# Performance work log

Measured on AMD Instinct MI355X. Metric: run time of the kernel, lower is better.

## Reference

```python
import jax, jax.numpy as jnp
import numpy as np

N_NODES = 100000
N_EDGES = 1600000
D = 128


def setup_inputs() -> dict:
    key = jax.random.key(0)
    ks = jax.random.split(key, 8)
    s = lambda fan_in: 1.0 / np.sqrt(fan_in)
    return {
        "node_feature": jax.random.normal(ks[0], (N_NODES, D), dtype=jnp.float32),
        "src": jax.random.randint(ks[1], (N_EDGES,), 0, N_NODES),
        "dst": jax.random.randint(ks[2], (N_EDGES,), 0, N_NODES),
        "W1": jax.random.normal(ks[3], (2 * D, D), dtype=jnp.float32) * s(2 * D),
        "b1": jnp.zeros((D,), dtype=jnp.float32),
        "W2": jax.random.normal(ks[4], (D, D), dtype=jnp.float32) * s(D),
        "b2": jnp.zeros((D,), dtype=jnp.float32),
        "W3": jax.random.normal(ks[5], (D, D), dtype=jnp.float32) * s(D),
        "b3": jnp.zeros((D,), dtype=jnp.float32),
    }


def reference(node_feature, src, dst, W1, b1, W2, b2, W3, b3):
    n_nodes = node_feature.shape[0]
    # message: gather src node features over edges  [E, D]
    msg = node_feature[src]
    # reduce: sum messages into destination nodes   [N, D]
    agg = jax.ops.segment_sum(msg, dst, num_segments=n_nodes)
    # apply: concat(aggregated, own) -> MLP         [N, 2D] -> [N, D]
    inp = jnp.concatenate([agg, node_feature], axis=-1)
    h = jax.nn.relu(inp @ W1 + b1)
    h = jax.nn.relu(h @ W2 + b2)
    return h @ W3 + b3
```

## Files before the change

kernel.cpp:

```cpp
#include <hip/hip_runtime.h>

#define NNODES 100000
#define NEDGES 1600000
#define DD 128
#define BM 32
#define NBUCK 98
#define NBLK_MLP (NNODES / BM)
#define CAP 32
#define CAPB 20480
#define BIN1_WGS 200
#define BIN1_EPW 8192

#define WS_GCUR 100000
#define WS_BBASE 100128
#define WS_OFFS 100352
#define WS_ESRC 201216

#define WT1HI 0
#define WT1LO 32768
#define WT2HI 65536
#define WT2LO 81920
#define WT3HI 98304
#define WT3LO 114688

typedef __attribute__((ext_vector_type(8))) short short8;
typedef __attribute__((ext_vector_type(4))) float f32x4;

__device__ __forceinline__ void bf16_split(float x, ushort& hi, ushort& lo) {
  unsigned u = __float_as_uint(x);
  ushort h = (ushort)((u + 0x7FFFu + ((u >> 16) & 1u)) >> 16);
  float r = x - __uint_as_float(((unsigned)h) << 16);
  unsigned v = __float_as_uint(r);
  ushort l = (ushort)((v + 0x7FFFu + ((v >> 16) & 1u)) >> 16);
  hi = h;
  lo = l;
}

__device__ __forceinline__ void split8(const float4 v0, const float4 v1,
                                       short8& hi, short8& lo) {
  float x[8] = {v0.x, v0.y, v0.z, v0.w, v1.x, v1.y, v1.z, v1.w};
#pragma unroll
  for (int j = 0; j < 8; ++j) {
    ushort h, l;
    bf16_split(x[j], h, l);
    hi[j] = (short)h;
    lo[j] = (short)l;
  }
}

__global__ __launch_bounds__(256) void bin1_kernel(const int* __restrict__ src,
                                                   const int* __restrict__ dst,
                                                   int* __restrict__ gcur,
                                                   unsigned* __restrict__ ebuf) {
  __shared__ unsigned stage[NBUCK][CAP];
  __shared__ int scnt[NBUCK];
  const int t = threadIdx.x;
  for (int i = t; i < NBUCK; i += 256) scnt[i] = 0;
  __syncthreads();
  const int e0 = blockIdx.x * BIN1_EPW;
  for (int r = 0; r < BIN1_EPW / 1024; ++r) {
    unsigned item[4];
    int buck[4];
    int pend[4];
#pragma unroll
    for (int j = 0; j < 4; ++j) {
      pend[j] = 0;
      int e = e0 + r * 1024 + j * 256 + t;
      if (e < NEDGES) {
        int d = dst[e];
        int s = src[e];
        buck[j] = d >> 10;
        item[j] = ((unsigned)(d & 1023) << 17) | (unsigned)s;
        int p = atomicAdd(&scnt[buck[j]], 1);
        if (p < CAP)
          stage[buck[j]][p] = item[j];
        else
          pend[j] = 1;
      }
    }
    int pendLeft;
    do {
      __syncthreads();
      if (t < NBUCK && scnt[t] >= CAP) {
        int base = t * CAPB + atomicAdd(&gcur[t], CAP);
        for (int q = 0; q < CAP; ++q) ebuf[base + q] = stage[t][q];
        scnt[t] = 0;
      }
      __syncthreads();
      int mypend = 0;
#pragma unroll
      for (int j = 0; j < 4; ++j) {
        if (pend[j]) {
          int p = atomicAdd(&scnt[buck[j]], 1);
          if (p < CAP) {
            stage[buck[j]][p] = item[j];
            pend[j] = 0;
          } else {
            mypend = 1;
          }
        }
      }
      pendLeft = __syncthreads_count(mypend);
    } while (pendLeft > 0);
  }
  __syncthreads();
  if (t < NBUCK) {
    int n = scnt[t];
    if (n > 0) {
      int base = t * CAPB + atomicAdd(&gcur[t], n);
      for (int q = 0; q < n; ++q) ebuf[base + q] = stage[t][q];
    }
  }
}

__global__ __launch_bounds__(128) void bscan_kernel(const int* __restrict__ gcur,
                                                    int* __restrict__ bbase,
                                                    int* __restrict__ offs) {
  __shared__ int s[128];
  const int t = threadIdx.x;
  int v = (t < NBUCK) ? gcur[t] : 0;
  s[t] = v;
  __syncthreads();
  for (int off = 1; off < 128; off <<= 1) {
    int u = (t >= off) ? s[t - off] : 0;
    __syncthreads();
    s[t] += u;
    __syncthreads();
  }
  if (t < NBUCK) bbase[t] = s[t] - v;
  if (t == NBUCK - 1) offs[NNODES] = s[t];
}

__global__ __launch_bounds__(1024) void bucket_csr_kernel(const unsigned* __restrict__ ebuf,
                                                          const int* __restrict__ gcur,
                                                          const int* __restrict__ bbase,
                                                          int* __restrict__ offs,
                                                          int* __restrict__ esrc) {
  __shared__ int h[1024];
  __shared__ int cur[1024];
  const int t = threadIdx.x;
  const int c = blockIdx.x;
  const int n = gcur[c];
  const unsigned* eb = ebuf + c * CAPB;
  h[t] = 0;
  __syncthreads();
  for (int i = t; i < n; i += 1024) atomicAdd(&h[eb[i] >> 17], 1);
  __syncthreads();
  int v = h[t];
  for (int off = 1; off < 1024; off <<= 1) {
    int u = (t >= off) ? h[t - off] : 0;
    __syncthreads();
    h[t] += u;
    __syncthreads();
  }
  int excl = h[t] - v + bbase[c];
  int node = (c << 10) + t;
  if (node < NNODES) offs[node] = excl;
  cur[t] = excl;
  __syncthreads();
  for (int i = t; i < n; i += 1024) {
    unsigned e = eb[i];
    int p = atomicAdd(&cur[e >> 17], 1);
    esrc[p] = (int)(e & 0x1FFFFu);
  }
}

__global__ __launch_bounds__(256) void wprep_kernel(const float* __restrict__ W1,
                                                    const float* __restrict__ W2,
                                                    const float* __restrict__ W3,
                                                    ushort* __restrict__ wt) {
  int tid = blockIdx.x * 256 + threadIdx.x;
  const float* W;
  int dstHi, dstLo, k, col;
  if (tid < 32768) {
    int j = tid & 7, l = (tid >> 3) & 63, tile = tid >> 9;
    int kk = tile & 7, c16 = tile >> 3;
    k = kk * 32 + (l >> 4) * 8 + j;
    col = c16 * 16 + (l & 15);
    W = W1;
    dstHi = WT1HI + tid;
    dstLo = WT1LO + tid;
  } else {
    int t2 = tid - 32768;
    int which = t2 >> 14;
    int t1 = t2 & 16383;
    int j = t1 & 7, l = (t1 >> 3) & 63, tile = t1 >> 9;
    int kk = tile & 3, c16 = tile >> 2;
    k = kk * 32 + (l >> 4) * 8 + j;
    col = c16 * 16 + (l & 15);
    W = which ? W3 : W2;
    dstHi = (which ? WT3HI : WT2HI) + t1;
    dstLo = (which ? WT3LO : WT2LO) + t1;
  }
  ushort hi, lo;
  bf16_split(W[k * DD + col], hi, lo);
  wt[dstHi] = hi;
  wt[dstLo] = lo;
}


template <int KT>
__device__ __forceinline__ void lds_ksteps(const ushort* Hh, const ushort* Hl,
                                           const ushort* __restrict__ WhiT,
                                           const ushort* __restrict__ WloT,
                                           int tileOff, int rb, int wc, int lane,
                                           int l15, int lhi, f32x4 acc[4]) {
#pragma unroll 2
  for (int kk = 0; kk < 4; ++kk) {
    int row = rb + l15;
    int byte = (row * 256 + kk * 64 + lhi * 16) ^ ((row & 7) << 4);
    short8 ahi = *(const short8*)((const char*)Hh + byte);
    short8 alo = *(const short8*)((const char*)Hl + byte);
#pragma unroll
    for (int ct = 0; ct < 4; ++ct) {
      int tb = ((wc * 4 + ct) * KT + tileOff + kk) * 512 + lane * 8;
      short8 bhi = *(const short8*)&WhiT[tb];
      short8 blo = *(const short8*)&WloT[tb];
      acc[ct] = __builtin_amdgcn_mfma_f32_16x16x32_bf16(ahi, bhi, acc[ct], 0, 0, 0);
      acc[ct] = __builtin_amdgcn_mfma_f32_16x16x32_bf16(ahi, blo, acc[ct], 0, 0, 0);
      acc[ct] = __builtin_amdgcn_mfma_f32_16x16x32_bf16(alo, bhi, acc[ct], 0, 0, 0);
    }
  }
}

__device__ __forceinline__ void l1_step(const float* __restrict__ srcb,
                                        const ushort* __restrict__ wt,
                                        int kkTile, int kOff, int rowA,
                                        int wc, int lane, int lhi,
                                        f32x4 acc[4]) {
  const float* p = srcb + rowA * DD + kOff + lhi * 8;
  float4 v0 = *(const float4*)p;
  float4 v1 = *(const float4*)(p + 4);
  short8 ahi, alo;
  split8(v0, v1, ahi, alo);
#pragma unroll
  for (int ct = 0; ct < 4; ++ct) {
    int tb = ((wc * 4 + ct) * 8 + kkTile) * 512 + lane * 8;
    short8 bhi = *(const short8*)&wt[WT1HI + tb];
    short8 blo = *(const short8*)&wt[WT1LO + tb];
    acc[ct] = __builtin_amdgcn_mfma_f32_16x16x32_bf16(ahi, bhi, acc[ct], 0, 0, 0);
    acc[ct] = __builtin_amdgcn_mfma_f32_16x16x32_bf16(ahi, blo, acc[ct], 0, 0, 0);
    acc[ct] = __builtin_amdgcn_mfma_f32_16x16x32_bf16(alo, bhi, acc[ct], 0, 0, 0);
  }
}

__device__ __forceinline__ void store_h(ushort* Hh, ushort* Hl,
                                        const float* __restrict__ b,
                                        int rb, int wc, int l15, int lhi,
                                        f32x4 acc[4]) {
#pragma unroll
  for (int ct = 0; ct < 4; ++ct) {
    int col = wc * 64 + ct * 16 + l15;
    float bias = b[col];
#pragma unroll
    for (int i = 0; i < 4; ++i) {
      int row = rb + lhi * 4 + i;
      float v = fmaxf(acc[ct][i] + bias, 0.f);
      ushort h, l;
      bf16_split(v, h, l);
      int byte = (row * 256 + col * 2) ^ ((row & 7) << 4);
      *(ushort*)((char*)Hh + byte) = h;
      *(ushort*)((char*)Hl + byte) = l;
    }
  }
}

__global__ __launch_bounds__(256, 8) void fused_kernel(const float* __restrict__ nf,
                                                       const int* __restrict__ offs,
                                                       const int* __restrict__ esrc,
                                                       const ushort* __restrict__ wt,
                                                       const float* __restrict__ b1,
                                                       const float* __restrict__ b2,
                                                       const float* __restrict__ b3,
                                                       float* __restrict__ out) {
  __shared__ ushort smem[8192];
  __shared__ int nextRow;
  ushort* Xhi = smem;
  ushort* Xlo = smem + 4096;

  const int t = threadIdx.x;
  const int lane = t & 63;
  const int w = t >> 6;
  const int rb = (w & 1) * 16;
  const int wc = w >> 1;
  const int l15 = lane & 15;
  const int lhi = lane >> 4;
  const int base = blockIdx.x * BM;

  if (t == 0) nextRow = 0;
  __syncthreads();

  {
    const int l32 = t & 31;
    const int col = l32 << 2;
    for (;;) {
      int r;
      if (l32 == 0) r = atomicAdd(&nextRow, 1);
      r = __shfl(r, 0, 32);
      if (r >= BM) break;
      const int node = base + r;
      float4 a0 = make_float4(0.f, 0.f, 0.f, 0.f);
      float4 a1 = make_float4(0.f, 0.f, 0.f, 0.f);
      float4 a2 = make_float4(0.f, 0.f, 0.f, 0.f);
      float4 a3 = make_float4(0.f, 0.f, 0.f, 0.f);
      const int beg = offs[node];
      const int end = offs[node + 1];
      int i = beg;
      int s0, s1, s2, s3;
      const bool have4 = (i + 3 < end);
      if (have4) {
        s0 = esrc[i]; s1 = esrc[i + 1]; s2 = esrc[i + 2]; s3 = esrc[i + 3];
      }
      for (; i + 7 < end; i += 4) {
        int n0 = esrc[i + 4], n1 = esrc[i + 5], n2 = esrc[i + 6], n3 = esrc[i + 7];
        float4 v0 = *(const float4*)&nf[s0 * DD + col];
        float4 v1 = *(const float4*)&nf[s1 * DD + col];
        float4 v2 = *(const float4*)&nf[s2 * DD + col];
        float4 v3 = *(const float4*)&nf[s3 * DD + col];
        a0.x += v0.x; a0.y += v0.y; a0.z += v0.z; a0.w += v0.w;
        a1.x += v1.x; a1.y += v1.y; a1.z += v1.z; a1.w += v1.w;
        a2.x += v2.x; a2.y += v2.y; a2.z += v2.z; a2.w += v2.w;
        a3.x += v3.x; a3.y += v3.y; a3.z += v3.z; a3.w += v3.w;
        s0 = n0; s1 = n1; s2 = n2; s3 = n3;
      }
      if (have4) {
        float4 v0 = *(const float4*)&nf[s0 * DD + col];
        float4 v1 = *(const float4*)&nf[s1 * DD + col];
        float4 v2 = *(const float4*)&nf[s2 * DD + col];
        float4 v3 = *(const float4*)&nf[s3 * DD + col];
        a0.x += v0.x; a0.y += v0.y; a0.z += v0.z; a0.w += v0.w;
        a1.x += v1.x; a1.y += v1.y; a1.z += v1.z; a1.w += v1.w;
        a2.x += v2.x; a2.y += v2.y; a2.z += v2.z; a2.w += v2.w;
        a3.x += v3.x; a3.y += v3.y; a3.z += v3.z; a3.w += v3.w;
        i += 4;
      }
      for (; i < end; ++i) {
        int s = esrc[i];
        float4 v0 = *(const float4*)&nf[s * DD + col];
        a0.x += v0.x; a0.y += v0.y; a0.z += v0.z; a0.w += v0.w;
      }
      a0.x += a1.x; a0.y += a1.y; a0.z += a1.z; a0.w += a1.w;
      a2.x += a3.x; a2.y += a3.y; a2.z += a3.z; a2.w += a3.w;
      a0.x += a2.x; a0.y += a2.y; a0.z += a2.z; a0.w += a2.w;
      ushort h0, h1, h2, h3, l0, l1, l2, l3;
      bf16_split(a0.x, h0, l0);
      bf16_split(a0.y, h1, l1);
      bf16_split(a0.z, h2, l2);
      bf16_split(a0.w, h3, l3);
      int byte = (r * 256 + col * 2) ^ ((r & 7) << 4);
      *(ushort4*)((char*)Xhi + byte) = make_ushort4(h0, h1, h2, h3);
      *(ushort4*)((char*)Xlo + byte) = make_ushort4(l0, l1, l2, l3);
    }
  }
  __syncthreads();

  const int rowG = base + rb + l15;
  const f32x4 z = {0.f, 0.f, 0.f, 0.f};
  f32x4 acc[4];

#pragma unroll
  for (int ct = 0; ct < 4; ++ct) acc[ct] = z;
  lds_ksteps<8>(Xhi, Xlo, wt + WT1HI, wt + WT1LO, 0, rb, wc, lane, l15, lhi, acc);
#pragma unroll 2
  for (int kk = 0; kk < 4; ++kk)
    l1_step(nf, wt, kk + 4, kk * 32, rowG, wc, lane, lhi, acc);
  __syncthreads();
  store_h(Xhi, Xlo, b1, rb, wc, l15, lhi, acc);
  __syncthreads();

#pragma unroll
  for (int ct = 0; ct < 4; ++ct) acc[ct] = z;
  lds_ksteps<4>(Xhi, Xlo, wt + WT2HI, wt + WT2LO, 0, rb, wc, lane, l15, lhi, acc);
  __syncthreads();
  store_h(Xhi, Xlo, b2, rb, wc, l15, lhi, acc);
  __syncthreads();

#pragma unroll
  for (int ct = 0; ct < 4; ++ct) acc[ct] = z;
  lds_ksteps<4>(Xhi, Xlo, wt + WT3HI, wt + WT3LO, 0, rb, wc, lane, l15, lhi, acc);
#pragma unroll
  for (int ct = 0; ct < 4; ++ct) {
    int col = wc * 64 + ct * 16 + l15;
    float bias = b3[col];
#pragma unroll
    for (int i = 0; i < 4; ++i) {
      int row = base + rb + lhi * 4 + i;
      out[row * DD + col] = acc[ct][i] + bias;
    }
  }
}

extern "C" void kernel_launch(void* const* d_in, const int* in_sizes, int n_in,
                              void* d_out, int out_size, void* d_ws, size_t ws_size,
                              hipStream_t stream) {
  const float* nf = (const float*)d_in[0];
  const int* src = (const int*)d_in[1];
  const int* dst = (const int*)d_in[2];
  const float* W1 = (const float*)d_in[3];
  const float* b1 = (const float*)d_in[4];
  const float* W2 = (const float*)d_in[5];
  const float* b2 = (const float*)d_in[6];
  const float* W3 = (const float*)d_in[7];
  const float* b3 = (const float*)d_in[8];
  float* out = (float*)d_out;

  int* wsi = (int*)d_ws;
  int* gcur = wsi + WS_GCUR;
  int* bbase = wsi + WS_BBASE;
  int* offs = wsi + WS_OFFS;
  int* esrc = wsi + WS_ESRC;
  ushort* wt = (ushort*)wsi;

  unsigned* ebuf = (unsigned*)out;

  hipMemsetAsync(gcur, 0, NBUCK * sizeof(int), stream);
  bin1_kernel<<<BIN1_WGS, 256, 0, stream>>>(src, dst, gcur, ebuf);
  bscan_kernel<<<1, 128, 0, stream>>>(gcur, bbase, offs);
  bucket_csr_kernel<<<NBUCK, 1024, 0, stream>>>(ebuf, gcur, bbase, offs, esrc);
  wprep_kernel<<<256, 256, 0, stream>>>(W1, W2, W3, wt);
  fused_kernel<<<NBLK_MLP, 256, 0, stream>>>(nf, offs, esrc, wt, b1, b2, b3, out);
}
```

Measured before the change: 250.6 us.

## Enlarge MLP row tile to 64 and restructure warp tiling for weight reuse

Doubles the fused kernel's node tile from 32 to 64 rows. Each warp now covers 4 row tiles by 2 column tiles instead of 1 by 4, so every weight fragment loaded from global memory feeds four row tiles and less weight traffic is spent per node. The atomic-based dynamic row assignment in the aggregation stage is replaced by a static 8-rows-per-half-warp split, with bounds checks for the partial last tile. The binning kernel's launch shape also changes. The larger LDS footprint and lower launch-bounds occupancy (5 instead of 8) may reduce latency hiding, and static row assignment gives up load balancing across nodes with uneven in-degree.

```diff
diff --git a/kernel.cpp b/kernel.cpp
--- a/kernel.cpp
+++ b/kernel.cpp
@@ -3,13 +3,13 @@
 #define NNODES 100000
 #define NEDGES 1600000
 #define DD 128
-#define BM 32
+#define BM 64
 #define NBUCK 98
-#define NBLK_MLP (NNODES / BM)
+#define NBLK_MLP ((NNODES + BM - 1) / BM)
 #define CAP 32
 #define CAPB 20480
-#define BIN1_WGS 200
-#define BIN1_EPW 8192
+#define BIN1_WGS 391
+#define BIN1_EPW 4096
 
 #define WS_GCUR 100000
 #define WS_BBASE 100128
@@ -203,69 +203,86 @@
 __device__ __forceinline__ void lds_ksteps(const ushort* Hh, const ushort* Hl,
                                            const ushort* __restrict__ WhiT,
                                            const ushort* __restrict__ WloT,
-                                           int tileOff, int rb, int wc, int lane,
-                                           int l15, int lhi, f32x4 acc[4]) {
+                                           int tileOff, int wc2, int lane,
+                                           int l15, int lhi, f32x4 acc[4][2]) {
 #pragma unroll 2
   for (int kk = 0; kk < 4; ++kk) {
-    int row = rb + l15;
-    int byte = (row * 256 + kk * 64 + lhi * 16) ^ ((row & 7) << 4);
-    short8 ahi = *(const short8*)((const char*)Hh + byte);
-    short8 alo = *(const short8*)((const char*)Hl + byte);
-#pragma unroll
-    for (int ct = 0; ct < 4; ++ct) {
-      int tb = ((wc * 4 + ct) * KT + tileOff + kk) * 512 + lane * 8;
-      short8 bhi = *(const short8*)&WhiT[tb];
-      short8 blo = *(const short8*)&WloT[tb];
-      acc[ct] = __builtin_amdgcn_mfma_f32_16x16x32_bf16(ahi, bhi, acc[ct], 0, 0, 0);
-      acc[ct] = __builtin_amdgcn_mfma_f32_16x16x32_bf16(ahi, blo, acc[ct], 0, 0, 0);
-      acc[ct] = __builtin_amdgcn_mfma_f32_16x16x32_bf16(alo, bhi, acc[ct], 0, 0, 0);
+    short8 bhi[2], blo[2];
+#pragma unroll
+    for (int ct = 0; ct < 2; ++ct) {
+      int tb = ((wc2 + ct) * KT + tileOff + kk) * 512 + lane * 8;
+      bhi[ct] = *(const short8*)&WhiT[tb];
+      blo[ct] = *(const short8*)&WloT[tb];
+    }
+#pragma unroll
+    for (int rt = 0; rt < 4; ++rt) {
+      int row = rt * 16 + l15;
+      int byte = (row * 256 + kk * 64 + lhi * 16) ^ ((row & 7) << 4);
+      short8 ahi = *(const short8*)((const char*)Hh + byte);
+      short8 alo = *(const short8*)((const char*)Hl + byte);
+#pragma unroll
+      for (int ct = 0; ct < 2; ++ct) {
+        acc[rt][ct] = __builtin_amdgcn_mfma_f32_16x16x32_bf16(ahi, bhi[ct], acc[rt][ct], 0, 0, 0);
+        acc[rt][ct] = __builtin_amdgcn_mfma_f32_16x16x32_bf16(ahi, blo[ct], acc[rt][ct], 0, 0, 0);
+        acc[rt][ct] = __builtin_amdgcn_mfma_f32_16x16x32_bf16(alo, bhi[ct], acc[rt][ct], 0, 0, 0);
+      }
     }
   }
 }
 
 __device__ __forceinline__ void l1_step(const float* __restrict__ srcb,
                                         const ushort* __restrict__ wt,
-                                        int kkTile, int kOff, int rowA,
-                                        int wc, int lane, int lhi,
-                                        f32x4 acc[4]) {
-  const float* p = srcb + rowA * DD + kOff + lhi * 8;
-  float4 v0 = *(const float4*)p;
-  float4 v1 = *(const float4*)(p + 4);
-  short8 ahi, alo;
-  split8(v0, v1, ahi, alo);
-#pragma unroll
-  for (int ct = 0; ct < 4; ++ct) {
-    int tb = ((wc * 4 + ct) * 8 + kkTile) * 512 + lane * 8;
-    short8 bhi = *(const short8*)&wt[WT1HI + tb];
-    short8 blo = *(const short8*)&wt[WT1LO + tb];
-    acc[ct] = __builtin_amdgcn_mfma_f32_16x16x32_bf16(ahi, bhi, acc[ct], 0, 0, 0);
-    acc[ct] = __builtin_amdgcn_mfma_f32_16x16x32_bf16(ahi, blo, acc[ct], 0, 0, 0);
-    acc[ct] = __builtin_amdgcn_mfma_f32_16x16x32_bf16(alo, bhi, acc[ct], 0, 0, 0);
+                                        int kkTile, int kOff, const int rowA[4],
+                                        int wc2, int lane, int lhi,
+                                        f32x4 acc[4][2]) {
+  short8 bhi[2], blo[2];
+#pragma unroll
+  for (int ct = 0; ct < 2; ++ct) {
+    int tb = ((wc2 + ct) * 8 + kkTile) * 512 + lane * 8;
+    bhi[ct] = *(const short8*)&wt[WT1HI + tb];
+    blo[ct] = *(const short8*)&wt[WT1LO + tb];
+  }
+#pragma unroll
+  for (int rt = 0; rt < 4; ++rt) {
+    const float* p = srcb + rowA[rt] * DD + kOff + lhi * 8;
+    float4 v0 = *(const float4*)p;
+    float4 v1 = *(const float4*)(p + 4);
+    short8 ahi, alo;
+    split8(v0, v1, ahi, alo);
+#pragma unroll
+    for (int ct = 0; ct < 2; ++ct) {
+      acc[rt][ct] = __builtin_amdgcn_mfma_f32_16x16x32_bf16(ahi, bhi[ct], acc[rt][ct], 0, 0, 0);
+      acc[rt][ct] = __builtin_amdgcn_mfma_f32_16x16x32_bf16(ahi, blo[ct], acc[rt][ct], 0, 0, 0);
+      acc[rt][ct] = __builtin_amdgcn_mfma_f32_16x16x32_bf16(alo, bhi[ct], acc[rt][ct], 0, 0, 0);
+    }
   }
 }
 
 __device__ __forceinline__ void store_h(ushort* Hh, ushort* Hl,
                                         const float* __restrict__ b,
-                                        int rb, int wc, int l15, int lhi,
-                                        f32x4 acc[4]) {
-#pragma unroll
-  for (int ct = 0; ct < 4; ++ct) {
-    int col = wc * 64 + ct * 16 + l15;
-    float bias = b[col];
-#pragma unroll
-    for (int i = 0; i < 4; ++i) {
-      int row = rb + lhi * 4 + i;
-      float v = fmaxf(acc[ct][i] + bias, 0.f);
-      ushort h, l;
-      bf16_split(v, h, l);
-      int byte = (row * 256 + col * 2) ^ ((row & 7) << 4);
-      *(ushort*)((char*)Hh + byte) = h;
-      *(ushort*)((char*)Hl + byte) = l;
-    }
-  }
-}
-
-__global__ __launch_bounds__(256, 8) void fused_kernel(const float* __restrict__ nf,
+                                        int wc2, int l15, int lhi,
+                                        f32x4 acc[4][2]) {
+#pragma unroll
+  for (int rt = 0; rt < 4; ++rt) {
+#pragma unroll
+    for (int ct = 0; ct < 2; ++ct) {
+      int col = (wc2 + ct) * 16 + l15;
+      float bias = b[col];
+#pragma unroll
+      for (int i = 0; i < 4; ++i) {
+        int row = rt * 16 + lhi * 4 + i;
+        float v = fmaxf(acc[rt][ct][i] + bias, 0.f);
+        ushort h, l;
+        bf16_split(v, h, l);
+        int byte = (row * 256 + col * 2) ^ ((row & 7) << 4);
+        *(ushort*)((char*)Hh + byte) = h;
+        *(ushort*)((char*)Hl + byte) = l;
+      }
+    }
+  }
+}
+
+__global__ __launch_bounds__(256, 5) void fused_kernel(const float* __restrict__ nf,
                                                        const int* __restrict__ offs,
                                                        const int* __restrict__ esrc,
                                                        const ushort* __restrict__ wt,
@@ -273,32 +290,26 @@
                                                        const float* __restrict__ b2,
                                                        const float* __restrict__ b3,
                                                        float* __restrict__ out) {
-  __shared__ ushort smem[8192];
-  __shared__ int nextRow;
+  __shared__ ushort smem[16384];
   ushort* Xhi = smem;
-  ushort* Xlo = smem + 4096;
+  ushort* Xlo = smem + 8192;
 
   const int t = threadIdx.x;
   const int lane = t & 63;
   const int w = t >> 6;
-  const int rb = (w & 1) * 16;
-  const int wc = w >> 1;
+  const int wc2 = w * 2;
   const int l15 = lane & 15;
   const int lhi = lane >> 4;
   const int base = blockIdx.x * BM;
 
-  if (t == 0) nextRow = 0;
-  __syncthreads();
-
   {
+    const int g = t >> 5;
     const int l32 = t & 31;
     const int col = l32 << 2;
-    for (;;) {
-      int r;
-      if (l32 == 0) r = atomicAdd(&nextRow, 1);
-      r = __shfl(r, 0, 32);
-      if (r >= BM) break;
+    for (int j = 0; j < 8; ++j) {
+      const int r = g * 8 + j;
       const int node = base + r;
+      if (node >= NNODES) break;
       float4 a0 = make_float4(0.f, 0.f, 0.f, 0.f);
       float4 a1 = make_float4(0.f, 0.f, 0.f, 0.f);
       float4 a2 = make_float4(0.f, 0.f, 0.f, 0.f);
@@ -354,38 +365,50 @@
   }
   __syncthreads();
 
-  const int rowG = base + rb + l15;
+  int rowA[4];
+#pragma unroll
+  for (int rt = 0; rt < 4; ++rt) rowA[rt] = min(base + rt * 16 + l15, NNODES - 1);
+
   const f32x4 z = {0.f, 0.f, 0.f, 0.f};
-  f32x4 acc[4];
-
-#pragma unroll
-  for (int ct = 0; ct < 4; ++ct) acc[ct] = z;
-  lds_ksteps<8>(Xhi, Xlo, wt + WT1HI, wt + WT1LO, 0, rb, wc, lane, l15, lhi, acc);
+  f32x4 acc[4][2];
+
+#pragma unroll
+  for (int rt = 0; rt < 4; ++rt)
+#pragma unroll
+    for (int ct = 0; ct < 2; ++ct) acc[rt][ct] = z;
+  lds_ksteps<8>(Xhi, Xlo, wt + WT1HI, wt + WT1LO, 0, wc2, lane, l15, lhi, acc);
 #pragma unroll 2
   for (int kk = 0; kk < 4; ++kk)
-    l1_step(nf, wt, kk + 4, kk * 32, rowG, wc, lane, lhi, acc);
-  __syncthreads();
-  store_h(Xhi, Xlo, b1, rb, wc, l15, lhi, acc);
-  __syncthreads();
-
-#pragma unroll
-  for (int ct = 0; ct < 4; ++ct) acc[ct] = z;
-  lds_ksteps<4>(Xhi, Xlo, wt + WT2HI, wt + WT2LO, 0, rb, wc, lane, l15, lhi, acc);
-  __syncthreads();
-  store_h(Xhi, Xlo, b2, rb, wc, l15, lhi, acc);
-  __syncthreads();
-
-#pragma unroll
-  for (int ct = 0; ct < 4; ++ct) acc[ct] = z;
-  lds_ksteps<4>(Xhi, Xlo, wt + WT3HI, wt + WT3LO, 0, rb, wc, lane, l15, lhi, acc);
-#pragma unroll
-  for (int ct = 0; ct < 4; ++ct) {
-    int col = wc * 64 + ct * 16 + l15;
-    float bias = b3[col];
-#pragma unroll
-    for (int i = 0; i < 4; ++i) {
-      int row = base + rb + lhi * 4 + i;
-      out[row * DD + col] = acc[ct][i] + bias;
+    l1_step(nf, wt, kk + 4, kk * 32, rowA, wc2, lane, lhi, acc);
+  __syncthreads();
+  store_h(Xhi, Xlo, b1, wc2, l15, lhi, acc);
+  __syncthreads();
+
+#pragma unroll
+  for (int rt = 0; rt < 4; ++rt)
+#pragma unroll
+    for (int ct = 0; ct < 2; ++ct) acc[rt][ct] = z;
+  lds_ksteps<4>(Xhi, Xlo, wt + WT2HI, wt + WT2LO, 0, wc2, lane, l15, lhi, acc);
+  __syncthreads();
+  store_h(Xhi, Xlo, b2, wc2, l15, lhi, acc);
+  __syncthreads();
+
+#pragma unroll
+  for (int rt = 0; rt < 4; ++rt)
+#pragma unroll
+    for (int ct = 0; ct < 2; ++ct) acc[rt][ct] = z;
+  lds_ksteps<4>(Xhi, Xlo, wt + WT3HI, wt + WT3LO, 0, wc2, lane, l15, lhi, acc);
+#pragma unroll
+  for (int rt = 0; rt < 4; ++rt) {
+#pragma unroll
+    for (int ct = 0; ct < 2; ++ct) {
+      int col = (wc2 + ct) * 16 + l15;
+      float bias = b3[col];
+#pragma unroll
+      for (int i = 0; i < 4; ++i) {
+        int row = base + rt * 16 + lhi * 4 + i;
+        if (row < NNODES) out[row * DD + col] = acc[rt][ct][i] + bias;
+      }
     }
   }
 }
```

Result: faster. 240.0 us (-4.3%).
